# Kernel optimization log

Hardware: AMD Instinct MI355X
Metric: run time of the kernel (lower is better)

## Reference

```python
import jax, jax.numpy as jnp
import numpy as np

EPS = 1e-06
N, K, O = 100000, 64, 1024


def setup_inputs() -> dict:
    key = jax.random.key(0)
    k1, k2, k3 = jax.random.split(key, 3)
    # counts: non-negative read counts per particle (scaled uniform, like count data)
    counts = jnp.floor(jax.random.uniform(k1, (N, O), dtype=jnp.float32) * 10.0)
    # otu_dist: K community profiles over O OTUs (simplex rows)
    otu_raw = jax.random.uniform(k2, (K, O), dtype=jnp.float32) + 1e-3
    otu_dist = otu_raw / otu_raw.sum(axis=-1, keepdims=True)
    # comm_dist: mixture weights over K communities (simplex)
    comm_raw = jax.random.uniform(k3, (K,), dtype=jnp.float32) + 1e-3
    comm_dist = comm_raw / comm_raw.sum()
    return {"counts": counts, "otu_dist": otu_dist, "comm_dist": comm_dist}


def reference(counts, otu_dist, comm_dist):
    # (counts[:,None,:] * log(otu_dist[None,:,:]+EPS)).sum(-1) == counts @ log(otu_dist+EPS).T
    # (N,K) per-particle per-community log-likelihood + log prior weight
    log_otu = jnp.log(otu_dist + EPS)                      # (K, O)
    logsumexpand = jnp.einsum('no,ko->nk', counts, log_otu) + jnp.log(comm_dist + EPS)[None, :]
    summand = jax.scipy.special.logsumexp(logsumexpand, axis=1)  # (N,)
    return summand.sum()
```

## Files before the change

### kernel.cpp

```cpp
#include <hip/hip_runtime.h>
#include <hip/hip_bf16.h>
#include <math.h>

#define NP 100000
#define KC 64
#define OD 1024
#define EPSF 1e-6f

#define ROWS_PER_BLOCK 128
#define NBLOCKS ((NP + ROWS_PER_BLOCK - 1) / ROWS_PER_BLOCK)
#define NT 32

typedef __attribute__((ext_vector_type(8))) short short8;
typedef __attribute__((ext_vector_type(4))) float f32x4;

#define WS_LOGW      0
#define WS_PARTIALS  256
#define WS_BSTAGE    8192

__device__ __forceinline__ unsigned short f32_bf16_rn(float f) {
  unsigned int u = __float_as_uint(f);
  unsigned int r = u + 0x7fffu + ((u >> 16) & 1u);
  return (unsigned short)(r >> 16);
}

__device__ __forceinline__ void gll16(const void* gsrc, void* lds) {
  __builtin_amdgcn_global_load_lds(
      (const __attribute__((address_space(1))) unsigned int*)gsrc,
      (__attribute__((address_space(3))) unsigned int*)lds, 16, 0, 0);
}

__global__ void prep_kernel(const float* __restrict__ otu,
                            const float* __restrict__ comm,
                            unsigned short* __restrict__ bstage,
                            float* __restrict__ logw) {
  int b = blockIdx.x;
  if (b < KC) {
    int c = b & 15, ct = b >> 4;
    for (int k = threadIdx.x; k < OD; k += blockDim.x) {
      float x = logf(otu[b * OD + k] + EPSF);
      unsigned short h = f32_bf16_rn(x);
      float hf = __uint_as_float(((unsigned int)h) << 16);
      unsigned short l = f32_bf16_rn(x - hf);
      int t = k >> 5, g = (k >> 3) & 3, kk = k & 7;
      size_t base = (size_t)t * 4096 + (size_t)ct * 512 + (size_t)(g * 16 + c) * 8 + kk;
      bstage[base] = h;
      bstage[base + 2048] = l;
    }
  } else {
    if (threadIdx.x < KC) logw[threadIdx.x] = logf(comm[threadIdx.x] + EPSF);
  }
}

__global__ __launch_bounds__(256, 3)
void ll_kernel(const float* __restrict__ counts,
               const unsigned short* __restrict__ bstage,
               const float* __restrict__ logw,
               double* __restrict__ partials) {
  __shared__ unsigned short bufB[2][4096];

  const int tid = threadIdx.x;
  const int wave = tid >> 6;
  const int lane = tid & 63;
  const int g = lane >> 4;
  const int c = lane & 15;
  const int rowBase = blockIdx.x * ROWS_PER_BLOCK + wave * 32;

  f32x4 acc[2][4];
#pragma unroll
  for (int i = 0; i < 2; ++i)
#pragma unroll
    for (int j = 0; j < 4; ++j)
      acc[i][j] = (f32x4){0.f, 0.f, 0.f, 0.f};

  int r0 = rowBase + c;      if (r0 >= NP) r0 = NP - 1;
  int r1 = rowBase + 16 + c; if (r1 >= NP) r1 = NP - 1;
  const float* pa0 = counts + (size_t)r0 * OD + g * 8;
  const float* pa1 = counts + (size_t)r1 * OD + g * 8;

  const unsigned short* sbase = bstage + (size_t)wave * 1024 + (size_t)lane * 8;
  unsigned short* dbase0 = &bufB[0][wave * 1024];
  unsigned short* dbase1 = &bufB[1][wave * 1024];

  gll16(sbase, dbase0);
  gll16(sbase + 512, dbase0 + 512);
  float4 a0lo = *(const float4*)(pa0);
  float4 a0hi = *(const float4*)(pa0 + 4);
  float4 a1lo = *(const float4*)(pa1);
  float4 a1hi = *(const float4*)(pa1 + 4);
  asm volatile("s_waitcnt vmcnt(0)" ::: "memory");
  __syncthreads();

  int cur = 0;
  for (int t = 0; t < NT; ++t) {
    const int tn = (t + 1 < NT) ? t + 1 : NT - 1;

    const unsigned short* src = sbase + (size_t)tn * 4096;
    unsigned short* dst = (cur == 0) ? dbase1 : dbase0;
    gll16(src, dst);
    gll16(src + 512, dst + 512);
    asm volatile("" ::: "memory");

    const int kon = tn * 32;
    float4 n0lo = *(const float4*)(pa0 + kon);
    float4 n0hi = *(const float4*)(pa0 + kon + 4);
    float4 n1lo = *(const float4*)(pa1 + kon);
    float4 n1hi = *(const float4*)(pa1 + kon + 4);

    const unsigned short* bb = &bufB[cur][0];
    short8 fbh[4], fbl[4];
#pragma unroll
    for (int ct = 0; ct < 4; ++ct) {
      fbh[ct] = *(const short8*)(bb + ct * 512 + lane * 8);
      fbl[ct] = *(const short8*)(bb + 2048 + ct * 512 + lane * 8);
    }

    union { unsigned int u[4]; short8 v; } ua0, ua1;
    ua0.u[0] = __builtin_amdgcn_perm(__float_as_uint(a0lo.y), __float_as_uint(a0lo.x), 0x07060302u);
    ua0.u[1] = __builtin_amdgcn_perm(__float_as_uint(a0lo.w), __float_as_uint(a0lo.z), 0x07060302u);
    ua0.u[2] = __builtin_amdgcn_perm(__float_as_uint(a0hi.y), __float_as_uint(a0hi.x), 0x07060302u);
    ua0.u[3] = __builtin_amdgcn_perm(__float_as_uint(a0hi.w), __float_as_uint(a0hi.z), 0x07060302u);
    ua1.u[0] = __builtin_amdgcn_perm(__float_as_uint(a1lo.y), __float_as_uint(a1lo.x), 0x07060302u);
    ua1.u[1] = __builtin_amdgcn_perm(__float_as_uint(a1lo.w), __float_as_uint(a1lo.z), 0x07060302u);
    ua1.u[2] = __builtin_amdgcn_perm(__float_as_uint(a1hi.y), __float_as_uint(a1hi.x), 0x07060302u);
    ua1.u[3] = __builtin_amdgcn_perm(__float_as_uint(a1hi.w), __float_as_uint(a1hi.z), 0x07060302u);

#pragma unroll
    for (int ct = 0; ct < 4; ++ct) {
      acc[0][ct] = __builtin_amdgcn_mfma_f32_16x16x32_bf16(ua0.v, fbh[ct], acc[0][ct], 0, 0, 0);
      acc[1][ct] = __builtin_amdgcn_mfma_f32_16x16x32_bf16(ua1.v, fbh[ct], acc[1][ct], 0, 0, 0);
      acc[0][ct] = __builtin_amdgcn_mfma_f32_16x16x32_bf16(ua0.v, fbl[ct], acc[0][ct], 0, 0, 0);
      acc[1][ct] = __builtin_amdgcn_mfma_f32_16x16x32_bf16(ua1.v, fbl[ct], acc[1][ct], 0, 0, 0);
    }

    asm volatile("s_waitcnt vmcnt(4)" ::: "memory");
    __builtin_amdgcn_s_barrier();

    a0lo = n0lo; a0hi = n0hi; a1lo = n1lo; a1hi = n1hi;
    cur ^= 1;
  }

  float lw[4];
#pragma unroll
  for (int ct = 0; ct < 4; ++ct) lw[ct] = logw[ct * 16 + c];

  double lsum = 0.0;
#pragma unroll
  for (int rt = 0; rt < 2; ++rt) {
#pragma unroll
    for (int r = 0; r < 4; ++r) {
      float v0 = acc[rt][0][r] + lw[0];
      float v1 = acc[rt][1][r] + lw[1];
      float v2 = acc[rt][2][r] + lw[2];
      float v3 = acc[rt][3][r] + lw[3];
      float m = fmaxf(fmaxf(v0, v1), fmaxf(v2, v3));
      m = fmaxf(m, __shfl_xor(m, 1));
      m = fmaxf(m, __shfl_xor(m, 2));
      m = fmaxf(m, __shfl_xor(m, 4));
      m = fmaxf(m, __shfl_xor(m, 8));
      float s = __expf(v0 - m) + __expf(v1 - m) + __expf(v2 - m) + __expf(v3 - m);
      s += __shfl_xor(s, 1);
      s += __shfl_xor(s, 2);
      s += __shfl_xor(s, 4);
      s += __shfl_xor(s, 8);
      float lse = m + __logf(s);
      int row = rowBase + rt * 16 + g * 4 + r;
      if (c == 0 && row < NP) lsum += (double)lse;
    }
  }
  lsum += __shfl_xor(lsum, 16);
  lsum += __shfl_xor(lsum, 32);

  __shared__ double wpart[4];
  if (lane == 0) wpart[wave] = lsum;
  __syncthreads();
  if (tid == 0) partials[blockIdx.x] = wpart[0] + wpart[1] + wpart[2] + wpart[3];
}

__global__ void finalize_kernel(const double* __restrict__ partials,
                                float* __restrict__ out) {
  double s = 0.0;
  for (int i = threadIdx.x; i < NBLOCKS; i += 256) s += partials[i];
  s += __shfl_xor(s, 1);
  s += __shfl_xor(s, 2);
  s += __shfl_xor(s, 4);
  s += __shfl_xor(s, 8);
  s += __shfl_xor(s, 16);
  s += __shfl_xor(s, 32);
  __shared__ double sp[4];
  int w = threadIdx.x >> 6, lane = threadIdx.x & 63;
  if (lane == 0) sp[w] = s;
  __syncthreads();
  if (threadIdx.x == 0) out[0] = (float)(sp[0] + sp[1] + sp[2] + sp[3]);
}

extern "C" void kernel_launch(void* const* d_in, const int* in_sizes, int n_in,
                              void* d_out, int out_size, void* d_ws, size_t ws_size,
                              hipStream_t stream) {
  const float* counts = (const float*)d_in[0];
  const float* otu    = (const float*)d_in[1];
  const float* comm   = (const float*)d_in[2];
  float* out = (float*)d_out;
  char* ws = (char*)d_ws;

  float* logw          = (float*)(ws + WS_LOGW);
  double* partials     = (double*)(ws + WS_PARTIALS);
  unsigned short* bst  = (unsigned short*)(ws + WS_BSTAGE);

  prep_kernel<<<KC + 1, 256, 0, stream>>>(otu, comm, bst, logw);
  ll_kernel<<<NBLOCKS, 256, 0, stream>>>(counts, bst, logw, partials);
  finalize_kernel<<<1, 256, 0, stream>>>(partials, out);
}
```

Measured before the change: 571.8 us.

## Double K-step per iteration and load counts in-iteration instead of prefetching

Each iteration now covers 64 K-values instead of 32, halving the iteration and barrier count. The B staging layout and LDS buffers double to match, with four async LDS loads per wave per step. The register prefetch of the next counts tile is removed: counts for the current step are loaded at the top of the iteration and used right away. Explicit vmcnt waits are replaced by a full __syncthreads, which may expose global-load latency that the old prefetch hid.

Result: slower. 585.1 us (+2.3%).

```diff
diff --git a/kernel.cpp b/kernel.cpp
--- a/kernel.cpp
+++ b/kernel.cpp
@@ -9,7 +9,7 @@
 
 #define ROWS_PER_BLOCK 128
 #define NBLOCKS ((NP + ROWS_PER_BLOCK - 1) / ROWS_PER_BLOCK)
-#define NT 32
+#define NT 16
 
 typedef __attribute__((ext_vector_type(8))) short short8;
 typedef __attribute__((ext_vector_type(4))) float f32x4;
@@ -42,10 +42,11 @@
       unsigned short h = f32_bf16_rn(x);
       float hf = __uint_as_float(((unsigned int)h) << 16);
       unsigned short l = f32_bf16_rn(x - hf);
-      int t = k >> 5, g = (k >> 3) & 3, kk = k & 7;
-      size_t base = (size_t)t * 4096 + (size_t)ct * 512 + (size_t)(g * 16 + c) * 8 + kk;
+      int t = k >> 6, kg = (k >> 5) & 1, g = (k >> 3) & 3, kk = k & 7;
+      size_t base = (size_t)t * 8192 + (size_t)kg * 2048 + (size_t)ct * 512
+                  + (size_t)(g * 16 + c) * 8 + kk;
       bstage[base] = h;
-      bstage[base + 2048] = l;
+      bstage[base + 4096] = l;
     }
   } else {
     if (threadIdx.x < KC) logw[threadIdx.x] = logf(comm[threadIdx.x] + EPSF);
@@ -57,7 +58,7 @@
                const unsigned short* __restrict__ bstage,
                const float* __restrict__ logw,
                double* __restrict__ partials) {
-  __shared__ unsigned short bufB[2][4096];
+  __shared__ unsigned short bufB[2][8192];
 
   const int tid = threadIdx.x;
   const int wave = tid >> 6;
@@ -78,65 +79,70 @@
   const float* pa0 = counts + (size_t)r0 * OD + g * 8;
   const float* pa1 = counts + (size_t)r1 * OD + g * 8;
 
-  const unsigned short* sbase = bstage + (size_t)wave * 1024 + (size_t)lane * 8;
-  unsigned short* dbase0 = &bufB[0][wave * 1024];
-  unsigned short* dbase1 = &bufB[1][wave * 1024];
-
-  gll16(sbase, dbase0);
-  gll16(sbase + 512, dbase0 + 512);
-  float4 a0lo = *(const float4*)(pa0);
-  float4 a0hi = *(const float4*)(pa0 + 4);
-  float4 a1lo = *(const float4*)(pa1);
-  float4 a1hi = *(const float4*)(pa1 + 4);
-  asm volatile("s_waitcnt vmcnt(0)" ::: "memory");
+  const unsigned short* sbase = bstage + (size_t)wave * 2048 + (size_t)lane * 8;
+
+  {
+    unsigned short* dst = &bufB[0][wave * 2048];
+    gll16(sbase, dst);
+    gll16(sbase + 512, dst + 512);
+    gll16(sbase + 1024, dst + 1024);
+    gll16(sbase + 1536, dst + 1536);
+  }
   __syncthreads();
 
   int cur = 0;
   for (int t = 0; t < NT; ++t) {
     const int tn = (t + 1 < NT) ? t + 1 : NT - 1;
 
-    const unsigned short* src = sbase + (size_t)tn * 4096;
-    unsigned short* dst = (cur == 0) ? dbase1 : dbase0;
-    gll16(src, dst);
-    gll16(src + 512, dst + 512);
-    asm volatile("" ::: "memory");
-
-    const int kon = tn * 32;
-    float4 n0lo = *(const float4*)(pa0 + kon);
-    float4 n0hi = *(const float4*)(pa0 + kon + 4);
-    float4 n1lo = *(const float4*)(pa1 + kon);
-    float4 n1hi = *(const float4*)(pa1 + kon + 4);
-
-    const unsigned short* bb = &bufB[cur][0];
-    short8 fbh[4], fbl[4];
-#pragma unroll
-    for (int ct = 0; ct < 4; ++ct) {
-      fbh[ct] = *(const short8*)(bb + ct * 512 + lane * 8);
-      fbl[ct] = *(const short8*)(bb + 2048 + ct * 512 + lane * 8);
-    }
-
-    union { unsigned int u[4]; short8 v; } ua0, ua1;
-    ua0.u[0] = __builtin_amdgcn_perm(__float_as_uint(a0lo.y), __float_as_uint(a0lo.x), 0x07060302u);
-    ua0.u[1] = __builtin_amdgcn_perm(__float_as_uint(a0lo.w), __float_as_uint(a0lo.z), 0x07060302u);
-    ua0.u[2] = __builtin_amdgcn_perm(__float_as_uint(a0hi.y), __float_as_uint(a0hi.x), 0x07060302u);
-    ua0.u[3] = __builtin_amdgcn_perm(__float_as_uint(a0hi.w), __float_as_uint(a0hi.z), 0x07060302u);
-    ua1.u[0] = __builtin_amdgcn_perm(__float_as_uint(a1lo.y), __float_as_uint(a1lo.x), 0x07060302u);
-    ua1.u[1] = __builtin_amdgcn_perm(__float_as_uint(a1lo.w), __float_as_uint(a1lo.z), 0x07060302u);
-    ua1.u[2] = __builtin_amdgcn_perm(__float_as_uint(a1hi.y), __float_as_uint(a1hi.x), 0x07060302u);
-    ua1.u[3] = __builtin_amdgcn_perm(__float_as_uint(a1hi.w), __float_as_uint(a1hi.z), 0x07060302u);
-
-#pragma unroll
-    for (int ct = 0; ct < 4; ++ct) {
-      acc[0][ct] = __builtin_amdgcn_mfma_f32_16x16x32_bf16(ua0.v, fbh[ct], acc[0][ct], 0, 0, 0);
-      acc[1][ct] = __builtin_amdgcn_mfma_f32_16x16x32_bf16(ua1.v, fbh[ct], acc[1][ct], 0, 0, 0);
-      acc[0][ct] = __builtin_amdgcn_mfma_f32_16x16x32_bf16(ua0.v, fbl[ct], acc[0][ct], 0, 0, 0);
-      acc[1][ct] = __builtin_amdgcn_mfma_f32_16x16x32_bf16(ua1.v, fbl[ct], acc[1][ct], 0, 0, 0);
-    }
-
-    asm volatile("s_waitcnt vmcnt(4)" ::: "memory");
-    __builtin_amdgcn_s_barrier();
-
-    a0lo = n0lo; a0hi = n0hi; a1lo = n1lo; a1hi = n1hi;
+    {
+      const unsigned short* src = sbase + (size_t)tn * 8192;
+      unsigned short* dst = &bufB[cur ^ 1][wave * 2048];
+      gll16(src, dst);
+      gll16(src + 512, dst + 512);
+      gll16(src + 1024, dst + 1024);
+      gll16(src + 1536, dst + 1536);
+    }
+
+    const float* a0p = pa0 + t * 64;
+    const float* a1p = pa1 + t * 64;
+    float4 A0[2][2], A1[2][2];
+#pragma unroll
+    for (int kg = 0; kg < 2; ++kg) {
+      A0[kg][0] = *(const float4*)(a0p + kg * 32);
+      A0[kg][1] = *(const float4*)(a0p + kg * 32 + 4);
+      A1[kg][0] = *(const float4*)(a1p + kg * 32);
+      A1[kg][1] = *(const float4*)(a1p + kg * 32 + 4);
+    }
+
+#pragma unroll
+    for (int kg = 0; kg < 2; ++kg) {
+      short8 fbh[4], fbl[4];
+#pragma unroll
+      for (int ct = 0; ct < 4; ++ct) {
+        fbh[ct] = *(const short8*)(&bufB[cur][kg * 2048 + ct * 512 + lane * 8]);
+        fbl[ct] = *(const short8*)(&bufB[cur][4096 + kg * 2048 + ct * 512 + lane * 8]);
+      }
+
+      union { unsigned int u[4]; short8 v; } ua0, ua1;
+      ua0.u[0] = __builtin_amdgcn_perm(__float_as_uint(A0[kg][0].y), __float_as_uint(A0[kg][0].x), 0x07060302u);
+      ua0.u[1] = __builtin_amdgcn_perm(__float_as_uint(A0[kg][0].w), __float_as_uint(A0[kg][0].z), 0x07060302u);
+      ua0.u[2] = __builtin_amdgcn_perm(__float_as_uint(A0[kg][1].y), __float_as_uint(A0[kg][1].x), 0x07060302u);
+      ua0.u[3] = __builtin_amdgcn_perm(__float_as_uint(A0[kg][1].w), __float_as_uint(A0[kg][1].z), 0x07060302u);
+      ua1.u[0] = __builtin_amdgcn_perm(__float_as_uint(A1[kg][0].y), __float_as_uint(A1[kg][0].x), 0x07060302u);
+      ua1.u[1] = __builtin_amdgcn_perm(__float_as_uint(A1[kg][0].w), __float_as_uint(A1[kg][0].z), 0x07060302u);
+      ua1.u[2] = __builtin_amdgcn_perm(__float_as_uint(A1[kg][1].y), __float_as_uint(A1[kg][1].x), 0x07060302u);
+      ua1.u[3] = __builtin_amdgcn_perm(__float_as_uint(A1[kg][1].w), __float_as_uint(A1[kg][1].z), 0x07060302u);
+
+#pragma unroll
+      for (int ct = 0; ct < 4; ++ct) {
+        acc[0][ct] = __builtin_amdgcn_mfma_f32_16x16x32_bf16(ua0.v, fbh[ct], acc[0][ct], 0, 0, 0);
+        acc[1][ct] = __builtin_amdgcn_mfma_f32_16x16x32_bf16(ua1.v, fbh[ct], acc[1][ct], 0, 0, 0);
+        acc[0][ct] = __builtin_amdgcn_mfma_f32_16x16x32_bf16(ua0.v, fbl[ct], acc[0][ct], 0, 0, 0);
+        acc[1][ct] = __builtin_amdgcn_mfma_f32_16x16x32_bf16(ua1.v, fbl[ct], acc[1][ct], 0, 0, 0);
+      }
+    }
+
+    __syncthreads();
     cur ^= 1;
   }
 
```
